# Performance work log

Measured on AMD Instinct MI355X. Metric: run time of the kernel, lower is better.

Reference implementation:

```python
import jax, jax.numpy as jnp
import numpy as np

HID, OUT, EMB, NL = 256, 128, 1024, 4
NR, NP_, NM = 16384, 40000, 30000
E = 200000
NTYPES = 3  # lin_nodes keys: protein, molecule, reaction


def setup_inputs() -> dict:
    key = jax.random.key(0)
    ks = jax.random.split(key, 32)
    f32 = jnp.float32
    inp = {}
    inp["x_reaction"] = jax.random.normal(ks[0], (NR, EMB), f32)
    inp["x_protein"] = jax.random.normal(ks[1], (NP_, EMB), f32)
    inp["x_molecule"] = jax.random.normal(ks[2], (NM, EMB), f32)
    inp["ei_p2r_src"] = jax.random.randint(ks[3], (E,), 0, NP_, jnp.int32)
    inp["ei_p2r_dst"] = jax.random.randint(ks[4], (E,), 0, NR, jnp.int32)
    inp["ei_m2r_src"] = jax.random.randint(ks[5], (E,), 0, NM, jnp.int32)
    inp["ei_m2r_dst"] = jax.random.randint(ks[6], (E,), 0, NR, jnp.int32)
    inp["ei_r2p_src"] = jax.random.randint(ks[7], (E,), 0, NR, jnp.int32)
    inp["ei_r2p_dst"] = jax.random.randint(ks[8], (E,), 0, NP_, jnp.int32)
    inp["ei_r2m_src"] = jax.random.randint(ks[9], (E,), 0, NR, jnp.int32)
    inp["ei_r2m_dst"] = jax.random.randint(ks[10], (E,), 0, NM, jnp.int32)
    inp["output_notes_opt"] = jax.random.normal(ks[11], (NR, EMB), f32)
    inp["output_types"] = jax.random.randint(ks[12], (NR,), 0, NTYPES, jnp.int32)
    s = 0.02
    # layer 0 SAGE params (lazy in_dim = EMB), one set per edge type (4 edge types)
    inp["Wl0"] = jax.random.normal(ks[13], (4, EMB, HID), f32) * s
    inp["Wr0"] = jax.random.normal(ks[14], (4, EMB, HID), f32) * s
    inp["bl0"] = jnp.zeros((4, HID), f32)
    # layers 1..3 SAGE params (in_dim = HID)
    inp["Wl"] = jax.random.normal(ks[15], (NL - 1, 4, HID, HID), f32) * s
    inp["Wr"] = jax.random.normal(ks[16], (NL - 1, 4, HID, HID), f32) * s
    inp["bl"] = jnp.zeros((NL - 1, 4, HID), f32)
    inp["W_reaction"] = jax.random.normal(ks[17], (HID, OUT), f32) * s
    inp["b_reaction"] = jnp.zeros((OUT,), f32)
    inp["W_nodes"] = jax.random.normal(ks[18], (NTYPES, EMB, OUT), f32) * s
    inp["b_nodes"] = jnp.zeros((NTYPES, OUT), f32)
    return inp


def _sage(x_src, x_dst, src, dst, n_dst, Wl, bl, Wr):
    # PyG SAGEConv (aggr='mean'): lin_l(mean_{j->i} x_j) + lin_r(x_i); lin_l has bias.
    g = x_src[src]                                              # [E, d] gather
    s = jax.ops.segment_sum(g, dst, num_segments=n_dst)          # [n_dst, d]
    cnt = jax.ops.segment_sum(jnp.ones((src.shape[0],), x_src.dtype), dst, num_segments=n_dst)
    mean = s / jnp.maximum(cnt, 1.0)[:, None]
    return mean @ Wl + bl + x_dst @ Wr


def _hetero_layer(xr, xp, xm, edges, Wl, bl, Wr):
    # HeteroConv(aggr='sum'): sum SAGE outputs per destination node type.
    (ps, pd), (ms, md), (rps, rpd), (rms, rmd) = edges
    new_r = (_sage(xp, xr, ps, pd, NR, Wl[0], bl[0], Wr[0])
             + _sage(xm, xr, ms, md, NR, Wl[1], bl[1], Wr[1]))
    new_p = _sage(xr, xp, rps, rpd, NP_, Wl[2], bl[2], Wr[2])
    new_m = _sage(xr, xm, rms, rmd, NM, Wl[3], bl[3], Wr[3])
    return new_r, new_p, new_m


def reference(x_reaction, x_protein, x_molecule,
              ei_p2r_src, ei_p2r_dst, ei_m2r_src, ei_m2r_dst,
              ei_r2p_src, ei_r2p_dst, ei_r2m_src, ei_r2m_dst,
              output_notes_opt, output_types,
              Wl0, bl0, Wr0, Wl, bl, Wr,
              W_reaction, b_reaction, W_nodes, b_nodes):
    edges = ((ei_p2r_src, ei_p2r_dst), (ei_m2r_src, ei_m2r_dst),
             (ei_r2p_src, ei_r2p_dst), (ei_r2m_src, ei_r2m_dst))
    xr, xp, xm = _hetero_layer(x_reaction, x_protein, x_molecule, edges, Wl0, bl0, Wr0)
    for l in range(NL - 1):
        xr, xp, xm = _hetero_layer(xr, xp, xm, edges, Wl[l], bl[l], Wr[l])
    reaction_out = xr @ W_reaction + b_reaction                  # [NR, OUT]
    # lin_nodes[t](v) per output node: project with all type linears, select by type id
    projs = jnp.einsum('ke,ted->ktd', output_notes_opt, W_nodes) + b_nodes[None]  # [NR, T, OUT]
    node_out = jnp.take_along_axis(projs, output_types[:, None, None].astype(jnp.int32), axis=1)[:, 0, :]
    # cosine similarity along dim=1, torch-style eps clamp on the norm product
    num = jnp.sum(reaction_out * node_out, axis=-1)
    den = jnp.maximum(jnp.linalg.norm(reaction_out, axis=-1) * jnp.linalg.norm(node_out, axis=-1), 1e-8)
    return (num / den + 1.0) * 0.5
```

## Files before the change

### kernel.cpp

```cpp
#include <hip/hip_runtime.h>
#include <math.h>
#include <stdint.h>

#define NR_ 16384
#define NP2_ 40000
#define NM_ 30000
#define NE_ 200000
#define EMB_ 1024
#define HID_ 256
#define OUTD_ 128

typedef __attribute__((ext_vector_type(8))) short bf16x8;
typedef __attribute__((ext_vector_type(4))) float f32x4;
typedef __attribute__((ext_vector_type(8))) unsigned short us8;

__device__ __forceinline__ unsigned short f2bf(float f) {
    uint32_t u = __builtin_bit_cast(uint32_t, f);
    u = (u + 0x7FFFu + ((u >> 16) & 1u)) >> 16;
    return (unsigned short)u;
}
__device__ __forceinline__ float bf2f(unsigned short u) {
    uint32_t v = ((uint32_t)u) << 16;
    return __builtin_bit_cast(float, v);
}

struct Csr4 {
    const int* src[4]; const int* dst[4];
    int* offs[4]; int* cur[4]; int* csr[4];
    int n[4];
};
__global__ void k_zero4(Csr4 c) {
    int y = blockIdx.y;
    int i = blockIdx.x * 256 + threadIdx.x;
    if (i < c.n[y]) c.cur[y][i] = 0;
}
__global__ void k_deg4(Csr4 c) {
    int y = blockIdx.y;
    int i = blockIdx.x * 256 + threadIdx.x;
    if (i < NE_) atomicAdd(&c.cur[y][c.dst[y][i]], 1);
}
__global__ void k_scanA(Csr4 c, int* __restrict__ csum) {
    int y = blockIdx.y;
    int n = c.n[y];
    int ch = blockIdx.x;
    int nch = (n + 1023) >> 10;
    if (ch >= nch) return;
    const int* deg = c.cur[y];
    int* offs = c.offs[y];
    __shared__ int ts[256];
    int base = ch << 10;
    int t = threadIdx.x;
    int v[4];
    int s = 0;
    #pragma unroll
    for (int k = 0; k < 4; ++k) {
        int i = base + t * 4 + k;
        v[k] = (i < n) ? deg[i] : 0;
        s += v[k];
    }
    ts[t] = s;
    __syncthreads();
    for (int st = 1; st < 256; st <<= 1) {
        int x = ts[t];
        int xo = (t >= st) ? ts[t - st] : 0;
        __syncthreads();
        ts[t] = x + xo;
        __syncthreads();
    }
    int run = (t > 0) ? ts[t - 1] : 0;
    #pragma unroll
    for (int k = 0; k < 4; ++k) {
        int i = base + t * 4 + k;
        if (i < n) offs[i] = run;
        run += v[k];
    }
    if (t == 255) csum[y * 40 + ch] = ts[255];
}
__global__ void k_scanB(Csr4 c, int* __restrict__ csum) {
    int y = threadIdx.x;
    if (y < 4) {
        int n = c.n[y];
        int nch = (n + 1023) >> 10;
        int acc = 0;
        for (int i = 0; i < nch; ++i) {
            int v = csum[y * 40 + i];
            csum[y * 40 + i] = acc;
            acc += v;
        }
        c.offs[y][n] = acc;
    }
}
__global__ void k_scanC(Csr4 c, const int* __restrict__ csum) {
    int y = blockIdx.y;
    int i = blockIdx.x * 256 + threadIdx.x;
    if (i < c.n[y]) {
        int v = c.offs[y][i] + csum[y * 40 + (i >> 10)];
        c.offs[y][i] = v;
        c.cur[y][i] = v;
    }
}
__global__ void k_scatter4(Csr4 c) {
    int y = blockIdx.y;
    int i = blockIdx.x * 256 + threadIdx.x;
    if (i < NE_) {
        int d = c.dst[y][i];
        int p = atomicAdd(&c.cur[y][d], 1);
        c.csr[y][p] = c.src[y][i];
    }
}

struct WItem { const float* a; const float* b; unsigned short* dst; int k; int n; };
struct WBatch { WItem it[32]; };
__global__ void k_wconvT(WBatch wb) {
    WItem w = wb.it[blockIdx.y];
    int total = w.k * w.n;
    int kmask = w.k - 1;
    int shift = (w.k == 1024) ? 10 : 8;
    for (int idx = blockIdx.x * 256 + threadIdx.x; idx < total; idx += gridDim.x * 256) {
        int k = idx & kmask, n = idx >> shift;
        float v = w.a[(size_t)k * w.n + n];
        if (w.b) v += w.b[(size_t)k * w.n + n];
        w.dst[idx] = f2bf(v);
    }
}

struct GSeg {
    const void* A; const unsigned short* Bt; void* C; const float* bias;
    int lda, ldc, M, K, ntn, blk0;
};
struct GBatch { GSeg s[3]; int b1, b2, tot; };

template <bool OBF, bool AF32>
__global__ __launch_bounds__(256, 3) void k_gemmb(GBatch gb) {
    __shared__ __align__(16) unsigned short As[128 * 64];
    __shared__ __align__(16) unsigned short Bs[128 * 64];
    const int tid = threadIdx.x;
    const int lane = tid & 63;
    int nwg = gb.tot;
    int o = blockIdx.x;
    int q = nwg >> 3, r = nwg & 7;
    int xcd = o & 7, j = o >> 3;
    int wg = (xcd < r ? xcd * (q + 1) : r * (q + 1) + (xcd - r) * q) + j;
    const int si = (wg >= gb.b1) + (wg >= gb.b2);
    const GSeg sg = gb.s[si];
    const int local = wg - sg.blk0;
    const int bm = (local / sg.ntn) * 128;
    const int bn = (local % sg.ntn) * 128;
    const int lda = sg.lda, ldc = sg.ldc, M = sg.M, K = sg.K;
    const unsigned short* __restrict__ Bt = sg.Bt;
    const float* __restrict__ bias = sg.bias;

    const int wave = tid >> 6;
    const int wr = (wave >> 1) * 64;
    const int wc = (wave & 1) * 64;
    const int frow = lane & 15;
    const int fkc = lane >> 4;
    f32x4 acc[4][4] = {};

    for (int k0 = 0; k0 < K; k0 += 64) {
        #pragma unroll
        for (int i = 0; i < 4; ++i) {
            int c = tid + i * 256;
            int row = c >> 3, kc = c & 7;
            int srck = k0 + ((kc ^ (row & 7)) << 3);
            int ga = min(bm + row, M - 1);
            if constexpr (AF32) {
                const float* Af = (const float*)sg.A + (size_t)ga * lda + srck;
                float4 a0 = *(const float4*)Af;
                float4 a1 = *(const float4*)(Af + 4);
                us8 oo;
                oo[0] = f2bf(a0.x); oo[1] = f2bf(a0.y); oo[2] = f2bf(a0.z); oo[3] = f2bf(a0.w);
                oo[4] = f2bf(a1.x); oo[5] = f2bf(a1.y); oo[6] = f2bf(a1.z); oo[7] = f2bf(a1.w);
                *(us8*)(As + (size_t)c * 8) = oo;
            } else {
                __builtin_amdgcn_global_load_lds(
                    (const __attribute__((address_space(1))) unsigned int*)((const unsigned short*)sg.A + (size_t)ga * lda + srck),
                    (__attribute__((address_space(3))) unsigned int*)(As + (size_t)c * 8), 16, 0, 0);
            }
            __builtin_amdgcn_global_load_lds(
                (const __attribute__((address_space(1))) unsigned int*)(Bt + (size_t)(bn + row) * K + srck),
                (__attribute__((address_space(3))) unsigned int*)(Bs + (size_t)c * 8), 16, 0, 0);
        }
        __syncthreads();
        #pragma unroll
        for (int kk = 0; kk < 2; ++kk) {
            bf16x8 af[4], bfr[4];
            #pragma unroll
            for (int m = 0; m < 4; ++m) {
                int row = wr + m * 16 + frow;
                int kc = kk * 4 + fkc;
                af[m] = *(const bf16x8*)(As + (size_t)((row << 3) + (kc ^ (row & 7))) * 8);
            }
            #pragma unroll
            for (int n = 0; n < 4; ++n) {
                int row = wc + n * 16 + frow;
                int kc = kk * 4 + fkc;
                bfr[n] = *(const bf16x8*)(Bs + (size_t)((row << 3) + (kc ^ (row & 7))) * 8);
            }
            #pragma unroll
            for (int m = 0; m < 4; ++m)
                #pragma unroll
                for (int n = 0; n < 4; ++n)
                    acc[m][n] = __builtin_amdgcn_mfma_f32_16x16x32_bf16(bfr[n], af[m], acc[m][n], 0, 0, 0);
        }
        __syncthreads();
    }

    const int ccol0 = (lane >> 4) << 2;
    #pragma unroll
    for (int m = 0; m < 4; ++m) {
        int row = bm + wr + m * 16 + frow;
        if (row < M) {
            #pragma unroll
            for (int n = 0; n < 4; ++n) {
                int col = bn + wc + n * 16 + ccol0;
                f32x4 v = acc[m][n];
                if (bias) {
                    v[0] += bias[col + 0];
                    v[1] += bias[col + 1];
                    v[2] += bias[col + 2];
                    v[3] += bias[col + 3];
                }
                if constexpr (OBF) {
                    ushort4 oo;
                    oo.x = f2bf(v[0]); oo.y = f2bf(v[1]); oo.z = f2bf(v[2]); oo.w = f2bf(v[3]);
                    *(ushort4*)((unsigned short*)sg.C + (size_t)row * ldc + col) = oo;
                } else {
                    *(float4*)((float*)sg.C + (size_t)row * ldc + col) = make_float4(v[0], v[1], v[2], v[3]);
                }
            }
        }
    }
}

__global__ __launch_bounds__(256) void k_aggw(const int* __restrict__ offs,
                                              const int* __restrict__ csr,
                                              const unsigned short* __restrict__ proj, int ldp,
                                              const float* __restrict__ bias,
                                              unsigned short* __restrict__ outx, int ldo,
                                              int ndst) {
    int node = blockIdx.x * 4 + (threadIdx.x >> 6);
    int lane = threadIdx.x & 63;
    if (node >= ndst) return;
    int beg = offs[node], end = offs[node + 1];
    float s0 = 0.f, s1 = 0.f, s2 = 0.f, s3 = 0.f;
    const unsigned short* base = proj + lane * 4;
    int e = beg;
    for (; e + 3 < end; e += 4) {
        int i0 = csr[e], i1 = csr[e + 1], i2 = csr[e + 2], i3 = csr[e + 3];
        ushort4 u0 = *(const ushort4*)(base + (size_t)i0 * ldp);
        ushort4 u1 = *(const ushort4*)(base + (size_t)i1 * ldp);
        ushort4 u2 = *(const ushort4*)(base + (size_t)i2 * ldp);
        ushort4 u3 = *(const ushort4*)(base + (size_t)i3 * ldp);
        s0 += bf2f(u0.x) + bf2f(u1.x) + bf2f(u2.x) + bf2f(u3.x);
        s1 += bf2f(u0.y) + bf2f(u1.y) + bf2f(u2.y) + bf2f(u3.y);
        s2 += bf2f(u0.z) + bf2f(u1.z) + bf2f(u2.z) + bf2f(u3.z);
        s3 += bf2f(u0.w) + bf2f(u1.w) + bf2f(u2.w) + bf2f(u3.w);
    }
    for (; e < end; ++e) {
        ushort4 u = *(const ushort4*)(base + (size_t)csr[e] * ldp);
        s0 += bf2f(u.x); s1 += bf2f(u.y); s2 += bf2f(u.z); s3 += bf2f(u.w);
    }
    float inv = 1.f / fmaxf((float)(end - beg), 1.f);
    float4 b4 = ((const float4*)bias)[lane];
    size_t o = (size_t)node * ldo + lane * 4;
    ushort4 cur = *(const ushort4*)(outx + o);
    ushort4 w;
    w.x = f2bf(bf2f(cur.x) + s0 * inv + b4.x);
    w.y = f2bf(bf2f(cur.y) + s1 * inv + b4.y);
    w.z = f2bf(bf2f(cur.z) + s2 * inv + b4.z);
    w.w = f2bf(bf2f(cur.w) + s3 * inv + b4.w);
    *(ushort4*)(outx + o) = w;
}

__global__ __launch_bounds__(256) void k_agg2w(const int* __restrict__ offsA,
                                               const int* __restrict__ csrA,
                                               const unsigned short* __restrict__ projA, int ldpA,
                                               const float* __restrict__ biasA,
                                               const int* __restrict__ offsB,
                                               const int* __restrict__ csrB,
                                               const unsigned short* __restrict__ projB, int ldpB,
                                               const float* __restrict__ biasB,
                                               unsigned short* __restrict__ outx, int ldo,
                                               int ndst) {
    int node = blockIdx.x * 4 + (threadIdx.x >> 6);
    int lane = threadIdx.x & 63;
    if (node >= ndst) return;
    float a0 = 0.f, a1 = 0.f, a2 = 0.f, a3 = 0.f;
    int begA = offsA[node], endA = offsA[node + 1];
    const unsigned short* baseA = projA + lane * 4;
    int e = begA;
    for (; e + 3 < endA; e += 4) {
        int i0 = csrA[e], i1 = csrA[e + 1], i2 = csrA[e + 2], i3 = csrA[e + 3];
        ushort4 u0 = *(const ushort4*)(baseA + (size_t)i0 * ldpA);
        ushort4 u1 = *(const ushort4*)(baseA + (size_t)i1 * ldpA);
        ushort4 u2 = *(const ushort4*)(baseA + (size_t)i2 * ldpA);
        ushort4 u3 = *(const ushort4*)(baseA + (size_t)i3 * ldpA);
        a0 += bf2f(u0.x) + bf2f(u1.x) + bf2f(u2.x) + bf2f(u3.x);
        a1 += bf2f(u0.y) + bf2f(u1.y) + bf2f(u2.y) + bf2f(u3.y);
        a2 += bf2f(u0.z) + bf2f(u1.z) + bf2f(u2.z) + bf2f(u3.z);
        a3 += bf2f(u0.w) + bf2f(u1.w) + bf2f(u2.w) + bf2f(u3.w);
    }
    for (; e < endA; ++e) {
        ushort4 u = *(const ushort4*)(baseA + (size_t)csrA[e] * ldpA);
        a0 += bf2f(u.x); a1 += bf2f(u.y); a2 += bf2f(u.z); a3 += bf2f(u.w);
    }
    float b0 = 0.f, b1 = 0.f, b2 = 0.f, b3 = 0.f;
    int begB = offsB[node], endB = offsB[node + 1];
    const unsigned short* baseB = projB + lane * 4;
    e = begB;
    for (; e + 3 < endB; e += 4) {
        int i0 = csrB[e], i1 = csrB[e + 1], i2 = csrB[e + 2], i3 = csrB[e + 3];
        ushort4 u0 = *(const ushort4*)(baseB + (size_t)i0 * ldpB);
        ushort4 u1 = *(const ushort4*)(baseB + (size_t)i1 * ldpB);
        ushort4 u2 = *(const ushort4*)(baseB + (size_t)i2 * ldpB);
        ushort4 u3 = *(const ushort4*)(baseB + (size_t)i3 * ldpB);
        b0 += bf2f(u0.x) + bf2f(u1.x) + bf2f(u2.x) + bf2f(u3.x);
        b1 += bf2f(u0.y) + bf2f(u1.y) + bf2f(u2.y) + bf2f(u3.y);
        b2 += bf2f(u0.z) + bf2f(u1.z) + bf2f(u2.z) + bf2f(u3.z);
        b3 += bf2f(u0.w) + bf2f(u1.w) + bf2f(u2.w) + bf2f(u3.w);
    }
    for (; e < endB; ++e) {
        ushort4 u = *(const ushort4*)(baseB + (size_t)csrB[e] * ldpB);
        b0 += bf2f(u.x); b1 += bf2f(u.y); b2 += bf2f(u.z); b3 += bf2f(u.w);
    }
    float invA = 1.f / fmaxf((float)(endA - begA), 1.f);
    float invB = 1.f / fmaxf((float)(endB - begB), 1.f);
    float4 bA = ((const float4*)biasA)[lane];
    float4 bB = ((const float4*)biasB)[lane];
    size_t o = (size_t)node * ldo + lane * 4;
    ushort4 cur = *(const ushort4*)(outx + o);
    ushort4 w;
    w.x = f2bf(bf2f(cur.x) + a0 * invA + bA.x + b0 * invB + bB.x);
    w.y = f2bf(bf2f(cur.y) + a1 * invA + bA.y + b1 * invB + bB.y);
    w.z = f2bf(bf2f(cur.z) + a2 * invA + bA.z + b2 * invB + bB.z);
    w.w = f2bf(bf2f(cur.w) + a3 * invA + bA.w + b3 * invB + bB.w);
    *(ushort4*)(outx + o) = w;
}

__global__ __launch_bounds__(256) void k_cos(const float* __restrict__ ro,
                                             const float* __restrict__ pr,
                                             const int* __restrict__ types,
                                             float* __restrict__ out, int nr) {
    int row = blockIdx.x * 4 + (threadIdx.x >> 6);
    int lane = threadIdx.x & 63;
    if (row >= nr) return;
    int t = types[row];
    float2 r = ((const float2*)(ro + (size_t)row * OUTD_))[lane];
    float2 nn = ((const float2*)(pr + (size_t)row * 384 + t * OUTD_))[lane];
    float num = r.x * nn.x + r.y * nn.y;
    float d1 = r.x * r.x + r.y * r.y;
    float d2 = nn.x * nn.x + nn.y * nn.y;
    #pragma unroll
    for (int s = 1; s < 64; s <<= 1) {
        num += __shfl_xor(num, s);
        d1 += __shfl_xor(d1, s);
        d2 += __shfl_xor(d2, s);
    }
    if (lane == 0) out[row] = (num / fmaxf(sqrtf(d1) * sqrtf(d2), 1e-8f) + 1.f) * 0.5f;
}

extern "C" void kernel_launch(void* const* d_in, const int* in_sizes, int n_in,
                              void* d_out, int out_size, void* d_ws, size_t ws_size,
                              hipStream_t stream) {
    const float* x_r0 = (const float*)d_in[0];
    const float* x_p0 = (const float*)d_in[1];
    const float* x_m0 = (const float*)d_in[2];
    const int* e_src[4] = {(const int*)d_in[3], (const int*)d_in[5], (const int*)d_in[7], (const int*)d_in[9]};
    const int* e_dst[4] = {(const int*)d_in[4], (const int*)d_in[6], (const int*)d_in[8], (const int*)d_in[10]};
    const float* notes = (const float*)d_in[11];
    const int* types = (const int*)d_in[12];
    const float* Wl0 = (const float*)d_in[13];
    const float* Wr0 = (const float*)d_in[14];
    const float* bl0 = (const float*)d_in[15];
    const float* WlL = (const float*)d_in[16];
    const float* WrL = (const float*)d_in[17];
    const float* blL = (const float*)d_in[18];
    const float* Wre = (const float*)d_in[19];
    const float* bre = (const float*)d_in[20];
    const float* Wn  = (const float*)d_in[21];
    const float* bn  = (const float*)d_in[22];
    float* out = (float*)d_out;

    uintptr_t base = (uintptr_t)d_ws;
    auto alloc = [&](size_t bytes) -> void* {
        uintptr_t p = (base + 255) & ~(uintptr_t)255;
        base = p + bytes;
        return (void*)p;
    };
    unsigned short* Rb[2] = {(unsigned short*)alloc((size_t)NR_ * 768 * 2),
                             (unsigned short*)alloc((size_t)NR_ * 768 * 2)};
    unsigned short* Pb[2] = {(unsigned short*)alloc((size_t)NP2_ * 512 * 2),
                             (unsigned short*)alloc((size_t)NP2_ * 512 * 2)};
    unsigned short* Mb[2] = {(unsigned short*)alloc((size_t)NM_ * 512 * 2),
                             (unsigned short*)alloc((size_t)NM_ * 512 * 2)};
    float* ro = (float*)alloc((size_t)NR_ * OUTD_ * 4);
    float* pr = (float*)alloc((size_t)NR_ * 384 * 4);
    unsigned short* wbf = (unsigned short*)alloc((size_t)4000000 * 2);
    int* csum = (int*)alloc(160 * 4);
    int nd[4] = {NR_, NR_, NP2_, NM_};
    Csr4 cs{};
    for (int t = 0; t < 4; ++t) {
        cs.src[t] = e_src[t]; cs.dst[t] = e_dst[t]; cs.n[t] = nd[t];
        cs.offs[t] = (int*)alloc(((size_t)nd[t] + 1) * 4);
        cs.cur[t]  = (int*)alloc((size_t)nd[t] * 4);
        cs.csr[t]  = (int*)alloc((size_t)NE_ * 4);
    }

    unsigned short *BR[4], *BP[4], *BM[4], *Bre, *Bn;
    {
        WBatch wb{};
        int cnt = 0;
        size_t woff = 0;
        auto add = [&](const float* a, const float* bb, int K, int N) -> unsigned short* {
            unsigned short* dst = wbf + woff;
            woff += (size_t)K * N;
            wb.it[cnt] = WItem{a, bb, dst, K, N};
            ++cnt;
            return dst;
        };
        const size_t w0 = (size_t)EMB_ * HID_;
        const size_t wl = (size_t)HID_ * HID_;
        for (int l = 0; l < 4; ++l) {
            int K = (l == 0) ? EMB_ : HID_;
            const float* Wr_ = (l == 0) ? Wr0 : WrL + (size_t)(l - 1) * 4 * wl;
            const float* Wl_ = (l == 0) ? Wl0 : WlL + (size_t)(l - 1) * 4 * wl;
            size_t ws_ = (l == 0) ? w0 : wl;
            BR[l] = add(Wr_ + 0 * ws_, Wr_ + 1 * ws_, K, HID_);
            add(Wl_ + 2 * ws_, nullptr, K, HID_);
            add(Wl_ + 3 * ws_, nullptr, K, HID_);
            BP[l] = add(Wr_ + 2 * ws_, nullptr, K, HID_);
            add(Wl_ + 0 * ws_, nullptr, K, HID_);
            BM[l] = add(Wr_ + 3 * ws_, nullptr, K, HID_);
            add(Wl_ + 1 * ws_, nullptr, K, HID_);
        }
        Bre = add(Wre, nullptr, HID_, OUTD_);
        Bn = add(Wn + 0 * (size_t)EMB_ * OUTD_, nullptr, EMB_, OUTD_);
        add(Wn + 1 * (size_t)EMB_ * OUTD_, nullptr, EMB_, OUTD_);
        add(Wn + 2 * (size_t)EMB_ * OUTD_, nullptr, EMB_, OUTD_);
        k_wconvT<<<dim3(128, cnt), 256, 0, stream>>>(wb);
    }

    k_zero4<<<dim3((NP2_ + 255) / 256, 4), 256, 0, stream>>>(cs);
    k_deg4<<<dim3((NE_ + 255) / 256, 4), 256, 0, stream>>>(cs);
    k_scanA<<<dim3(40, 4), 256, 0, stream>>>(cs, csum);
    k_scanB<<<1, 64, 0, stream>>>(cs, csum);
    k_scanC<<<dim3((NP2_ + 255) / 256, 4), 256, 0, stream>>>(cs, csum);
    k_scatter4<<<dim3((NE_ + 255) / 256, 4), 256, 0, stream>>>(cs);

    const int MT_R = (NR_ + 127) / 128;
    const int MT_P = (NP2_ + 127) / 128;
    const int MT_M = (NM_ + 127) / 128;
    auto seg = [](const void* A, const unsigned short* Bt, void* C, const float* bias,
                  int lda, int ldc, int M, int K, int ntn, int blk0) -> GSeg {
        return GSeg{A, Bt, C, bias, lda, ldc, M, K, ntn, blk0};
    };

    for (int l = 0; l < 4; ++l) {
        int K = (l == 0) ? EMB_ : HID_;
        unsigned short* R = Rb[l & 1];
        unsigned short* P = Pb[l & 1];
        unsigned short* M = Mb[l & 1];
        const float* bl_ = (l == 0) ? bl0 : blL + (size_t)(l - 1) * 4 * HID_;

        GBatch gb{};
        int nR = MT_R * 6, nP = MT_P * 4, nM = MT_M * 4;
        if (l == 0) {
            gb.s[0] = seg(x_r0, BR[0], R, nullptr, EMB_, 768, NR_, EMB_, 6, 0);
            gb.s[1] = seg(x_p0, BP[0], P, nullptr, EMB_, 512, NP2_, EMB_, 4, nR);
            gb.s[2] = seg(x_m0, BM[0], M, nullptr, EMB_, 512, NM_, EMB_, 4, nR + nP);
        } else {
            gb.s[0] = seg(Rb[(l - 1) & 1], BR[l], R, nullptr, 768, 768, NR_, K, 6, 0);
            gb.s[1] = seg(Pb[(l - 1) & 1], BP[l], P, nullptr, 512, 512, NP2_, K, 4, nR);
            gb.s[2] = seg(Mb[(l - 1) & 1], BM[l], M, nullptr, 512, 512, NM_, K, 4, nR + nP);
        }
        gb.b1 = nR; gb.b2 = nR + nP; gb.tot = nR + nP + nM;
        if (l == 0) k_gemmb<true, true><<<gb.tot, 256, 0, stream>>>(gb);
        else        k_gemmb<true, false><<<gb.tot, 256, 0, stream>>>(gb);

        k_agg2w<<<(NR_ + 3) / 4, 256, 0, stream>>>(cs.offs[0], cs.csr[0], P + 256, 512, bl_ + 0 * HID_,
                                                   cs.offs[1], cs.csr[1], M + 256, 512, bl_ + 1 * HID_,
                                                   R, 768, NR_);
        k_aggw<<<(NP2_ + 3) / 4, 256, 0, stream>>>(cs.offs[2], cs.csr[2], R + 256, 768, bl_ + 2 * HID_, P, 512, NP2_);
        k_aggw<<<(NM_ + 3) / 4, 256, 0, stream>>>(cs.offs[3], cs.csr[3], R + 512, 768, bl_ + 3 * HID_, M, 512, NM_);
    }

    {
        GBatch g1{};
        g1.s[0] = seg(Rb[1], Bre, ro, bre, 768, OUTD_, NR_, HID_, 1, 0);
        g1.b1 = g1.b2 = g1.tot = MT_R * 1;
        k_gemmb<false, false><<<g1.tot, 256, 0, stream>>>(g1);
        GBatch g2{};
        g2.s[0] = seg(notes, Bn, pr, bn, EMB_, 384, NR_, EMB_, 3, 0);
        g2.b1 = g2.b2 = g2.tot = MT_R * 3;
        k_gemmb<false, true><<<g2.tot, 256, 0, stream>>>(g2);
    }
    k_cos<<<NR_ / 4, 256, 0, stream>>>(ro, pr, types, out, NR_);
}
```

Measured before the change: 805.5 us.

## Batch aggregation kernels into one launch and merge final projection GEMMs

Replaces the three per-layer aggregation launches (one two-source, two single-source) with a single batched kernel that dispatches by block range to one of three segments. The two final GEMMs (reaction head and node-type projections) become one launch through a new kernel that picks fp32 or bf16 A-loading per segment at runtime. The GEMM launch bound goes from 3 to 4 waves per SIMD. The aim is less launch overhead and better fill at kernel tails. The cost is a runtime branch on A type inside the GEMM loop and possible register pressure from the tighter occupancy bound.

```diff
diff --git a/kernel.cpp b/kernel.cpp
--- a/kernel.cpp
+++ b/kernel.cpp
@@ -126,12 +126,12 @@
 
 struct GSeg {
     const void* A; const unsigned short* Bt; void* C; const float* bias;
-    int lda, ldc, M, K, ntn, blk0;
+    int lda, ldc, M, K, ntn, blk0, af32;
 };
 struct GBatch { GSeg s[3]; int b1, b2, tot; };
 
 template <bool OBF, bool AF32>
-__global__ __launch_bounds__(256, 3) void k_gemmb(GBatch gb) {
+__global__ __launch_bounds__(256, 4) void k_gemmb(GBatch gb) {
     __shared__ __align__(16) unsigned short As[128 * 64];
     __shared__ __align__(16) unsigned short Bs[128 * 64];
     const int tid = threadIdx.x;
@@ -233,109 +233,183 @@
     }
 }
 
-__global__ __launch_bounds__(256) void k_aggw(const int* __restrict__ offs,
-                                              const int* __restrict__ csr,
-                                              const unsigned short* __restrict__ proj, int ldp,
-                                              const float* __restrict__ bias,
-                                              unsigned short* __restrict__ outx, int ldo,
-                                              int ndst) {
-    int node = blockIdx.x * 4 + (threadIdx.x >> 6);
+__global__ __launch_bounds__(256, 4) void k_gemmf(GBatch gb) {
+    __shared__ __align__(16) unsigned short As[128 * 64];
+    __shared__ __align__(16) unsigned short Bs[128 * 64];
+    const int tid = threadIdx.x;
+    const int lane = tid & 63;
+    int nwg = gb.tot;
+    int o = blockIdx.x;
+    int q = nwg >> 3, r = nwg & 7;
+    int xcd = o & 7, j = o >> 3;
+    int wg = (xcd < r ? xcd * (q + 1) : r * (q + 1) + (xcd - r) * q) + j;
+    const int si = (wg >= gb.b1) + (wg >= gb.b2);
+    const GSeg sg = gb.s[si];
+    const int local = wg - sg.blk0;
+    const int bm = (local / sg.ntn) * 128;
+    const int bn = (local % sg.ntn) * 128;
+    const int lda = sg.lda, ldc = sg.ldc, M = sg.M, K = sg.K;
+    const unsigned short* __restrict__ Bt = sg.Bt;
+    const float* __restrict__ bias = sg.bias;
+
+    const int wave = tid >> 6;
+    const int wr = (wave >> 1) * 64;
+    const int wc = (wave & 1) * 64;
+    const int frow = lane & 15;
+    const int fkc = lane >> 4;
+    f32x4 acc[4][4] = {};
+
+    for (int k0 = 0; k0 < K; k0 += 64) {
+        #pragma unroll
+        for (int i = 0; i < 4; ++i) {
+            int c = tid + i * 256;
+            int row = c >> 3, kc = c & 7;
+            int srck = k0 + ((kc ^ (row & 7)) << 3);
+            int ga = min(bm + row, M - 1);
+            if (sg.af32) {
+                const float* Af = (const float*)sg.A + (size_t)ga * lda + srck;
+                float4 a0 = *(const float4*)Af;
+                float4 a1 = *(const float4*)(Af + 4);
+                us8 oo;
+                oo[0] = f2bf(a0.x); oo[1] = f2bf(a0.y); oo[2] = f2bf(a0.z); oo[3] = f2bf(a0.w);
+                oo[4] = f2bf(a1.x); oo[5] = f2bf(a1.y); oo[6] = f2bf(a1.z); oo[7] = f2bf(a1.w);
+                *(us8*)(As + (size_t)c * 8) = oo;
+            } else {
+                __builtin_amdgcn_global_load_lds(
+                    (const __attribute__((address_space(1))) unsigned int*)((const unsigned short*)sg.A + (size_t)ga * lda + srck),
+                    (__attribute__((address_space(3))) unsigned int*)(As + (size_t)c * 8), 16, 0, 0);
+            }
+            __builtin_amdgcn_global_load_lds(
+                (const __attribute__((address_space(1))) unsigned int*)(Bt + (size_t)(bn + row) * K + srck),
+                (__attribute__((address_space(3))) unsigned int*)(Bs + (size_t)c * 8), 16, 0, 0);
+        }
+        __syncthreads();
+        #pragma unroll
+        for (int kk = 0; kk < 2; ++kk) {
+            bf16x8 af[4], bfr[4];
+            #pragma unroll
+            for (int m = 0; m < 4; ++m) {
+                int row = wr + m * 16 + frow;
+                int kc = kk * 4 + fkc;
+                af[m] = *(const bf16x8*)(As + (size_t)((row << 3) + (kc ^ (row & 7))) * 8);
+            }
+            #pragma unroll
+            for (int n = 0; n < 4; ++n) {
+                int row = wc + n * 16 + frow;
+                int kc = kk * 4 + fkc;
+                bfr[n] = *(const bf16x8*)(Bs + (size_t)((row << 3) + (kc ^ (row & 7))) * 8);
+            }
+            #pragma unroll
+            for (int m = 0; m < 4; ++m)
+                #pragma unroll
+                for (int n = 0; n < 4; ++n)
+                    acc[m][n] = __builtin_amdgcn_mfma_f32_16x16x32_bf16(bfr[n], af[m], acc[m][n], 0, 0, 0);
+        }
+        __syncthreads();
+    }
+
+    const int ccol0 = (lane >> 4) << 2;
+    #pragma unroll
+    for (int m = 0; m < 4; ++m) {
+        int row = bm + wr + m * 16 + frow;
+        if (row < M) {
+            #pragma unroll
+            for (int n = 0; n < 4; ++n) {
+                int col = bn + wc + n * 16 + ccol0;
+                f32x4 v = acc[m][n];
+                v[0] += bias[col + 0];
+                v[1] += bias[col + 1];
+                v[2] += bias[col + 2];
+                v[3] += bias[col + 3];
+                *(float4*)((float*)sg.C + (size_t)row * ldc + col) = make_float4(v[0], v[1], v[2], v[3]);
+            }
+        }
+    }
+}
+
+struct ASeg {
+    const int* offsA; const int* csrA; const unsigned short* projA; int ldpA; const float* biasA;
+    const int* offsB; const int* csrB; const unsigned short* projB; int ldpB; const float* biasB;
+    unsigned short* outx; int ldo; int ndst; int blk0;
+};
+struct ABatch { ASeg s[3]; int b1, b2; };
+
+__global__ __launch_bounds__(256) void k_aggb(ABatch ab) {
+    int b = blockIdx.x;
+    int si = (b >= ab.b1) + (b >= ab.b2);
+    const ASeg sg = ab.s[si];
+    int node = (b - sg.blk0) * 4 + (threadIdx.x >> 6);
     int lane = threadIdx.x & 63;
-    if (node >= ndst) return;
-    int beg = offs[node], end = offs[node + 1];
-    float s0 = 0.f, s1 = 0.f, s2 = 0.f, s3 = 0.f;
-    const unsigned short* base = proj + lane * 4;
-    int e = beg;
-    for (; e + 3 < end; e += 4) {
-        int i0 = csr[e], i1 = csr[e + 1], i2 = csr[e + 2], i3 = csr[e + 3];
-        ushort4 u0 = *(const ushort4*)(base + (size_t)i0 * ldp);
-        ushort4 u1 = *(const ushort4*)(base + (size_t)i1 * ldp);
-        ushort4 u2 = *(const ushort4*)(base + (size_t)i2 * ldp);
-        ushort4 u3 = *(const ushort4*)(base + (size_t)i3 * ldp);
-        s0 += bf2f(u0.x) + bf2f(u1.x) + bf2f(u2.x) + bf2f(u3.x);
-        s1 += bf2f(u0.y) + bf2f(u1.y) + bf2f(u2.y) + bf2f(u3.y);
-        s2 += bf2f(u0.z) + bf2f(u1.z) + bf2f(u2.z) + bf2f(u3.z);
-        s3 += bf2f(u0.w) + bf2f(u1.w) + bf2f(u2.w) + bf2f(u3.w);
-    }
-    for (; e < end; ++e) {
-        ushort4 u = *(const ushort4*)(base + (size_t)csr[e] * ldp);
-        s0 += bf2f(u.x); s1 += bf2f(u.y); s2 += bf2f(u.z); s3 += bf2f(u.w);
-    }
-    float inv = 1.f / fmaxf((float)(end - beg), 1.f);
-    float4 b4 = ((const float4*)bias)[lane];
-    size_t o = (size_t)node * ldo + lane * 4;
-    ushort4 cur = *(const ushort4*)(outx + o);
+    if (node >= sg.ndst) return;
+
+    float a0 = 0.f, a1 = 0.f, a2 = 0.f, a3 = 0.f;
+    int begA = sg.offsA[node], endA = sg.offsA[node + 1];
+    {
+        const unsigned short* baseA = sg.projA + lane * 4;
+        const int* csrA = sg.csrA;
+        int ldpA = sg.ldpA;
+        int e = begA;
+        for (; e + 3 < endA; e += 4) {
+            int i0 = csrA[e], i1 = csrA[e + 1], i2 = csrA[e + 2], i3 = csrA[e + 3];
+            ushort4 u0 = *(const ushort4*)(baseA + (size_t)i0 * ldpA);
+            ushort4 u1 = *(const ushort4*)(baseA + (size_t)i1 * ldpA);
+            ushort4 u2 = *(const ushort4*)(baseA + (size_t)i2 * ldpA);
+            ushort4 u3 = *(const ushort4*)(baseA + (size_t)i3 * ldpA);
+            a0 += bf2f(u0.x) + bf2f(u1.x) + bf2f(u2.x) + bf2f(u3.x);
+            a1 += bf2f(u0.y) + bf2f(u1.y) + bf2f(u2.y) + bf2f(u3.y);
+            a2 += bf2f(u0.z) + bf2f(u1.z) + bf2f(u2.z) + bf2f(u3.z);
+            a3 += bf2f(u0.w) + bf2f(u1.w) + bf2f(u2.w) + bf2f(u3.w);
+        }
+        for (; e < endA; ++e) {
+            ushort4 u = *(const ushort4*)(baseA + (size_t)csrA[e] * ldpA);
+            a0 += bf2f(u.x); a1 += bf2f(u.y); a2 += bf2f(u.z); a3 += bf2f(u.w);
+        }
+    }
+    float invA = 1.f / fmaxf((float)(endA - begA), 1.f);
+    float4 bA = ((const float4*)sg.biasA)[lane];
+    float r0 = a0 * invA + bA.x;
+    float r1 = a1 * invA + bA.y;
+    float r2 = a2 * invA + bA.z;
+    float r3 = a3 * invA + bA.w;
+
+    if (sg.csrB) {
+        float b0 = 0.f, b1 = 0.f, b2 = 0.f, b3 = 0.f;
+        int begB = sg.offsB[node], endB = sg.offsB[node + 1];
+        const unsigned short* baseB = sg.projB + lane * 4;
+        const int* csrB = sg.csrB;
+        int ldpB = sg.ldpB;
+        int e = begB;
+        for (; e + 3 < endB; e += 4) {
+            int i0 = csrB[e], i1 = csrB[e + 1], i2 = csrB[e + 2], i3 = csrB[e + 3];
+            ushort4 u0 = *(const ushort4*)(baseB + (size_t)i0 * ldpB);
+            ushort4 u1 = *(const ushort4*)(baseB + (size_t)i1 * ldpB);
+            ushort4 u2 = *(const ushort4*)(baseB + (size_t)i2 * ldpB);
+            ushort4 u3 = *(const ushort4*)(baseB + (size_t)i3 * ldpB);
+            b0 += bf2f(u0.x) + bf2f(u1.x) + bf2f(u2.x) + bf2f(u3.x);
+            b1 += bf2f(u0.y) + bf2f(u1.y) + bf2f(u2.y) + bf2f(u3.y);
+            b2 += bf2f(u0.z) + bf2f(u1.z) + bf2f(u2.z) + bf2f(u3.z);
+            b3 += bf2f(u0.w) + bf2f(u1.w) + bf2f(u2.w) + bf2f(u3.w);
+        }
+        for (; e < endB; ++e) {
+            ushort4 u = *(const ushort4*)(baseB + (size_t)csrB[e] * ldpB);
+            b0 += bf2f(u.x); b1 += bf2f(u.y); b2 += bf2f(u.z); b3 += bf2f(u.w);
+        }
+        float invB = 1.f / fmaxf((float)(endB - begB), 1.f);
+        float4 bB = ((const float4*)sg.biasB)[lane];
+        r0 += b0 * invB + bB.x;
+        r1 += b1 * invB + bB.y;
+        r2 += b2 * invB + bB.z;
+        r3 += b3 * invB + bB.w;
+    }
+
+    size_t o = (size_t)node * sg.ldo + lane * 4;
+    ushort4 cur = *(const ushort4*)(sg.outx + o);
     ushort4 w;
-    w.x = f2bf(bf2f(cur.x) + s0 * inv + b4.x);
-    w.y = f2bf(bf2f(cur.y) + s1 * inv + b4.y);
-    w.z = f2bf(bf2f(cur.z) + s2 * inv + b4.z);
-    w.w = f2bf(bf2f(cur.w) + s3 * inv + b4.w);
-    *(ushort4*)(outx + o) = w;
-}
-
-__global__ __launch_bounds__(256) void k_agg2w(const int* __restrict__ offsA,
-                                               const int* __restrict__ csrA,
-                                               const unsigned short* __restrict__ projA, int ldpA,
-                                               const float* __restrict__ biasA,
-                                               const int* __restrict__ offsB,
-                                               const int* __restrict__ csrB,
-                                               const unsigned short* __restrict__ projB, int ldpB,
-                                               const float* __restrict__ biasB,
-                                               unsigned short* __restrict__ outx, int ldo,
-                                               int ndst) {
-    int node = blockIdx.x * 4 + (threadIdx.x >> 6);
-    int lane = threadIdx.x & 63;
-    if (node >= ndst) return;
-    float a0 = 0.f, a1 = 0.f, a2 = 0.f, a3 = 0.f;
-    int begA = offsA[node], endA = offsA[node + 1];
-    const unsigned short* baseA = projA + lane * 4;
-    int e = begA;
-    for (; e + 3 < endA; e += 4) {
-        int i0 = csrA[e], i1 = csrA[e + 1], i2 = csrA[e + 2], i3 = csrA[e + 3];
-        ushort4 u0 = *(const ushort4*)(baseA + (size_t)i0 * ldpA);
-        ushort4 u1 = *(const ushort4*)(baseA + (size_t)i1 * ldpA);
-        ushort4 u2 = *(const ushort4*)(baseA + (size_t)i2 * ldpA);
-        ushort4 u3 = *(const ushort4*)(baseA + (size_t)i3 * ldpA);
-        a0 += bf2f(u0.x) + bf2f(u1.x) + bf2f(u2.x) + bf2f(u3.x);
-        a1 += bf2f(u0.y) + bf2f(u1.y) + bf2f(u2.y) + bf2f(u3.y);
-        a2 += bf2f(u0.z) + bf2f(u1.z) + bf2f(u2.z) + bf2f(u3.z);
-        a3 += bf2f(u0.w) + bf2f(u1.w) + bf2f(u2.w) + bf2f(u3.w);
-    }
-    for (; e < endA; ++e) {
-        ushort4 u = *(const ushort4*)(baseA + (size_t)csrA[e] * ldpA);
-        a0 += bf2f(u.x); a1 += bf2f(u.y); a2 += bf2f(u.z); a3 += bf2f(u.w);
-    }
-    float b0 = 0.f, b1 = 0.f, b2 = 0.f, b3 = 0.f;
-    int begB = offsB[node], endB = offsB[node + 1];
-    const unsigned short* baseB = projB + lane * 4;
-    e = begB;
-    for (; e + 3 < endB; e += 4) {
-        int i0 = csrB[e], i1 = csrB[e + 1], i2 = csrB[e + 2], i3 = csrB[e + 3];
-        ushort4 u0 = *(const ushort4*)(baseB + (size_t)i0 * ldpB);
-        ushort4 u1 = *(const ushort4*)(baseB + (size_t)i1 * ldpB);
-        ushort4 u2 = *(const ushort4*)(baseB + (size_t)i2 * ldpB);
-        ushort4 u3 = *(const ushort4*)(baseB + (size_t)i3 * ldpB);
-        b0 += bf2f(u0.x) + bf2f(u1.x) + bf2f(u2.x) + bf2f(u3.x);
-        b1 += bf2f(u0.y) + bf2f(u1.y) + bf2f(u2.y) + bf2f(u3.y);
-        b2 += bf2f(u0.z) + bf2f(u1.z) + bf2f(u2.z) + bf2f(u3.z);
-        b3 += bf2f(u0.w) + bf2f(u1.w) + bf2f(u2.w) + bf2f(u3.w);
-    }
-    for (; e < endB; ++e) {
-        ushort4 u = *(const ushort4*)(baseB + (size_t)csrB[e] * ldpB);
-        b0 += bf2f(u.x); b1 += bf2f(u.y); b2 += bf2f(u.z); b3 += bf2f(u.w);
-    }
-    float invA = 1.f / fmaxf((float)(endA - begA), 1.f);
-    float invB = 1.f / fmaxf((float)(endB - begB), 1.f);
-    float4 bA = ((const float4*)biasA)[lane];
-    float4 bB = ((const float4*)biasB)[lane];
-    size_t o = (size_t)node * ldo + lane * 4;
-    ushort4 cur = *(const ushort4*)(outx + o);
-    ushort4 w;
-    w.x = f2bf(bf2f(cur.x) + a0 * invA + bA.x + b0 * invB + bB.x);
-    w.y = f2bf(bf2f(cur.y) + a1 * invA + bA.y + b1 * invB + bB.y);
-    w.z = f2bf(bf2f(cur.z) + a2 * invA + bA.z + b2 * invB + bB.z);
-    w.w = f2bf(bf2f(cur.w) + a3 * invA + bA.w + b3 * invB + bB.w);
-    *(ushort4*)(outx + o) = w;
+    w.x = f2bf(bf2f(cur.x) + r0);
+    w.y = f2bf(bf2f(cur.y) + r1);
+    w.z = f2bf(bf2f(cur.z) + r2);
+    w.w = f2bf(bf2f(cur.w) + r3);
+    *(ushort4*)(sg.outx + o) = w;
 }
 
 __global__ __launch_bounds__(256) void k_cos(const float* __restrict__ ro,
@@ -452,9 +526,11 @@
     const int MT_P = (NP2_ + 127) / 128;
     const int MT_M = (NM_ + 127) / 128;
     auto seg = [](const void* A, const unsigned short* Bt, void* C, const float* bias,
-                  int lda, int ldc, int M, int K, int ntn, int blk0) -> GSeg {
-        return GSeg{A, Bt, C, bias, lda, ldc, M, K, ntn, blk0};
+                  int lda, int ldc, int M, int K, int ntn, int blk0, int af32) -> GSeg {
+        return GSeg{A, Bt, C, bias, lda, ldc, M, K, ntn, blk0, af32};
     };
+
+    const int AB_R = (NR_ + 3) / 4, AB_P = (NP2_ + 3) / 4, AB_M = (NM_ + 3) / 4;
 
     for (int l = 0; l < 4; ++l) {
         int K = (l == 0) ? EMB_ : HID_;
@@ -466,34 +542,39 @@
         GBatch gb{};
         int nR = MT_R * 6, nP = MT_P * 4, nM = MT_M * 4;
         if (l == 0) {
-            gb.s[0] = seg(x_r0, BR[0], R, nullptr, EMB_, 768, NR_, EMB_, 6, 0);
-            gb.s[1] = seg(x_p0, BP[0], P, nullptr, EMB_, 512, NP2_, EMB_, 4, nR);
-            gb.s[2] = seg(x_m0, BM[0], M, nullptr, EMB_, 512, NM_, EMB_, 4, nR + nP);
+            gb.s[0] = seg(x_r0, BR[0], R, nullptr, EMB_, 768, NR_, EMB_, 6, 0, 1);
+            gb.s[1] = seg(x_p0, BP[0], P, nullptr, EMB_, 512, NP2_, EMB_, 4, nR, 1);
+            gb.s[2] = seg(x_m0, BM[0], M, nullptr, EMB_, 512, NM_, EMB_, 4, nR + nP, 1);
         } else {
-            gb.s[0] = seg(Rb[(l - 1) & 1], BR[l], R, nullptr, 768, 768, NR_, K, 6, 0);
-            gb.s[1] = seg(Pb[(l - 1) & 1], BP[l], P, nullptr, 512, 512, NP2_, K, 4, nR);
-            gb.s[2] = seg(Mb[(l - 1) & 1], BM[l], M, nullptr, 512, 512, NM_, K, 4, nR + nP);
+            gb.s[0] = seg(Rb[(l - 1) & 1], BR[l], R, nullptr, 768, 768, NR_, K, 6, 0, 0);
+            gb.s[1] = seg(Pb[(l - 1) & 1], BP[l], P, nullptr, 512, 512, NP2_, K, 4, nR, 0);
+            gb.s[2] = seg(Mb[(l - 1) & 1], BM[l], M, nullptr, 512, 512, NM_, K, 4, nR + nP, 0);
         }
         gb.b1 = nR; gb.b2 = nR + nP; gb.tot = nR + nP + nM;
         if (l == 0) k_gemmb<true, true><<<gb.tot, 256, 0, stream>>>(gb);
         else        k_gemmb<true, false><<<gb.tot, 256, 0, stream>>>(gb);
 
-        k_agg2w<<<(NR_ + 3) / 4, 256, 0, stream>>>(cs.offs[0], cs.csr[0], P + 256, 512, bl_ + 0 * HID_,
-                                                   cs.offs[1], cs.csr[1], M + 256, 512, bl_ + 1 * HID_,
-                                                   R, 768, NR_);
-        k_aggw<<<(NP2_ + 3) / 4, 256, 0, stream>>>(cs.offs[2], cs.csr[2], R + 256, 768, bl_ + 2 * HID_, P, 512, NP2_);
-        k_aggw<<<(NM_ + 3) / 4, 256, 0, stream>>>(cs.offs[3], cs.csr[3], R + 512, 768, bl_ + 3 * HID_, M, 512, NM_);
+        ABatch ab{};
+        ab.s[0] = ASeg{cs.offs[0], cs.csr[0], P + 256, 512, bl_ + 0 * HID_,
+                       cs.offs[1], cs.csr[1], M + 256, 512, bl_ + 1 * HID_,
+                       R, 768, NR_, 0};
+        ab.s[1] = ASeg{cs.offs[2], cs.csr[2], R + 256, 768, bl_ + 2 * HID_,
+                       nullptr, nullptr, nullptr, 0, nullptr,
+                       P, 512, NP2_, AB_R};
+        ab.s[2] = ASeg{cs.offs[3], cs.csr[3], R + 512, 768, bl_ + 3 * HID_,
+                       nullptr, nullptr, nullptr, 0, nullptr,
+                       M, 512, NM_, AB_R + AB_P};
+        ab.b1 = AB_R; ab.b2 = AB_R + AB_P;
+        k_aggb<<<AB_R + AB_P + AB_M, 256, 0, stream>>>(ab);
     }
 
     {
-        GBatch g1{};
-        g1.s[0] = seg(Rb[1], Bre, ro, bre, 768, OUTD_, NR_, HID_, 1, 0);
-        g1.b1 = g1.b2 = g1.tot = MT_R * 1;
-        k_gemmb<false, false><<<g1.tot, 256, 0, stream>>>(g1);
-        GBatch g2{};
-        g2.s[0] = seg(notes, Bn, pr, bn, EMB_, 384, NR_, EMB_, 3, 0);
-        g2.b1 = g2.b2 = g2.tot = MT_R * 3;
-        k_gemmb<false, true><<<g2.tot, 256, 0, stream>>>(g2);
+        GBatch gf{};
+        gf.s[0] = seg(Rb[1], Bre, ro, bre, 768, OUTD_, NR_, HID_, 1, 0, 0);
+        gf.s[1] = seg(notes, Bn, pr, bn, EMB_, 384, NR_, EMB_, 3, MT_R, 1);
+        gf.s[2] = gf.s[1];
+        gf.b1 = MT_R; gf.b2 = MT_R + MT_R * 3; gf.tot = MT_R + MT_R * 3;
+        k_gemmf<<<gf.tot, 256, 0, stream>>>(gf);
     }
     k_cos<<<NR_ / 4, 256, 0, stream>>>(ro, pr, types, out, NR_);
 }
```

Measured after the change: 834.2 us. 3.6% more time.
